# Kernel optimization log

Measured on AMD Instinct MI355X. Metric: run time of the kernel, lower is better.

## Reference

```python
import jax, jax.numpy as jnp
import numpy as np

HEADS = 8
DIM_HEAD = 64
SLICE = 64
DIM = 128
INNER = HEADS * DIM_HEAD
B, H, W = 4, 128, 128


def _conv(x_nchw, w_oihw, b):
    y = jax.lax.conv_general_dilated(
        x_nchw, w_oihw, window_strides=(1, 1), padding='SAME',
        dimension_numbers=('NCHW', 'OIHW', 'NCHW'))
    return y + b[None, :, None, None]


def setup_inputs() -> dict:
    key = jax.random.key(0)
    ks = jax.random.split(key, 10)
    s = lambda fan: 1.0 / np.sqrt(fan)
    return {
        'x': jax.random.normal(ks[0], (B, H, W, DIM), jnp.float32),
        'temperature': jnp.ones((1, HEADS, 1, 1), jnp.float32) * 0.5,
        'Wx': jax.random.normal(ks[1], (INNER, DIM, 3, 3), jnp.float32) * s(DIM * 9),
        'bx': jnp.zeros((INNER,), jnp.float32),
        'Wfx': jax.random.normal(ks[2], (INNER, DIM, 3, 3), jnp.float32) * s(DIM * 9),
        'bfx': jnp.zeros((INNER,), jnp.float32),
        'Ws': jax.random.normal(ks[3], (SLICE, DIM_HEAD), jnp.float32) * s(DIM_HEAD),
        'bs': jnp.zeros((SLICE,), jnp.float32),
        'Wq': jax.random.normal(ks[4], (DIM_HEAD, DIM_HEAD), jnp.float32) * s(DIM_HEAD),
        'Wk': jax.random.normal(ks[5], (DIM_HEAD, DIM_HEAD), jnp.float32) * s(DIM_HEAD),
        'Wv': jax.random.normal(ks[6], (DIM_HEAD, DIM_HEAD), jnp.float32) * s(DIM_HEAD),
        'Wo': jax.random.normal(ks[7], (DIM, INNER), jnp.float32) * s(INNER),
        'bo': jnp.zeros((DIM,), jnp.float32),
    }


def reference(x, temperature, Wx, bx, Wfx, bfx, Ws, bs, Wq, Wk, Wv, Wo, bo):
    b, h, w, _ = x.shape
    n = h * w
    scale = DIM_HEAD ** -0.5
    x_nchw = jnp.transpose(x, (0, 3, 1, 2))
    # conv projections -> [B, heads, N, dim_head]
    def to_heads(y):
        y = jnp.transpose(y, (0, 2, 3, 1)).reshape(b, n, HEADS, DIM_HEAD)
        return jnp.transpose(y, (0, 2, 1, 3))
    fx_mid = to_heads(_conv(x_nchw, Wfx, bfx))
    x_mid = to_heads(_conv(x_nchw, Wx, bx))
    # slice routing: softmax over M, temperature-scaled
    temp = jnp.clip(temperature, 0.1, 5.0)  # [1,heads,1,1]
    logits = (jnp.einsum('bhnc,gc->bhng', x_mid, Ws) + bs) / temp
    slice_weights = jax.nn.softmax(logits, axis=-1)  # [B,h,N,M]
    slice_norm = slice_weights.sum(axis=2)  # [B,h,M]
    slice_token = jnp.einsum('bhnc,bhng->bhgc', fx_mid, slice_weights)
    slice_token = slice_token / (slice_norm + 1e-5)[..., None]
    # small M x M attention over slice tokens
    q = jnp.einsum('bhgc,dc->bhgd', slice_token, Wq)
    k = jnp.einsum('bhgc,dc->bhgd', slice_token, Wk)
    v = jnp.einsum('bhgc,dc->bhgd', slice_token, Wv)
    dots = jnp.einsum('bhgd,bhkd->bhgk', q, k) * scale
    attn = jax.nn.softmax(dots, axis=-1)
    out_slice = jnp.einsum('bhgk,bhkd->bhgd', attn, v)
    # scatter back to points
    out_x = jnp.einsum('bhgc,bhng->bhnc', out_slice, slice_weights)
    out_x = jnp.transpose(out_x, (0, 2, 1, 3)).reshape(b, h, w, INNER)
    return jnp.einsum('bhwi,oi->bhwo', out_x, Wo) + bo
```

## Files before the change

### kernel.cpp

```cpp
#include <hip/hip_runtime.h>
#include <hip/hip_bf16.h>
#include <math.h>

#define B_ 4
#define H_ 128
#define W_ 128
#define DIM_ 128
#define HEADS_ 8
#define DH_ 64
#define G_ 64
#define INNER_ 512
#define N_ 16384

typedef __attribute__((ext_vector_type(8))) short sh8;
typedef __attribute__((ext_vector_type(4))) float vf4;

#define XPT_SLAB 4160
#define XPT_PLANE 2163200
#define WT_PLANE 1179648

__device__ __forceinline__ void gload16(const void* g, void* l) {
  __builtin_amdgcn_global_load_lds((const __attribute__((address_space(1))) void*)g,
                                   (__attribute__((address_space(3))) void*)l, 16, 0, 0);
}

__device__ __forceinline__ void split_bf16(float v, ushort& h, ushort& l) {
  __hip_bfloat16 hb = __float2bfloat16(v);
  float hf = __bfloat162float(hb);
  __hip_bfloat16 lb = __float2bfloat16(v - hf);
  h = *reinterpret_cast<ushort*>(&hb);
  l = *reinterpret_cast<ushort*>(&lb);
}

__global__ __launch_bounds__(256) void pad_tile_kernel(const float* __restrict__ x,
                                                       ushort* __restrict__ xpth,
                                                       ushort* __restrict__ xptl) {
  const int bz = blockIdx.y;
  x += (size_t)bz * N_ * DIM_;
  xpth += (size_t)bz * XPT_PLANE;
  xptl += (size_t)bz * XPT_PLANE;
  const int idx = blockIdx.x * 256 + threadIdx.x;
  const int row = idx / (4 * XPT_SLAB);
  const int rem = idx % (4 * XPT_SLAB);
  const int c0i = rem / XPT_SLAB;
  const int t2 = rem % XPT_SLAB;
  const int tile = t2 >> 3, j = t2 & 7;
  const int kg = tile / 130, px = tile % 130;
  const int c = c0i * 32 + kg * 8 + j;
  float v = 0.0f;
  if (row >= 1 && row <= H_ && px >= 1 && px <= W_)
    v = x[((size_t)(row - 1) * W_ + (px - 1)) * DIM_ + c];
  ushort hh, ll;
  split_bf16(v, hh, ll);
  xpth[idx] = hh;
  xptl[idx] = ll;
}

__global__ __launch_bounds__(256) void wfx_kernel(const float* __restrict__ Wfx,
                                                  ushort* __restrict__ wth,
                                                  ushort* __restrict__ wtl) {
  int idx = blockIdx.x * 256 + threadIdx.x;
  if (idx >= 9 * 512 * DIM_) return;
  const int c = idx & 127;
  const int ocf = (idx >> 7) & 511;
  const int tap = idx >> 16;
  float v = Wfx[((size_t)ocf * DIM_ + c) * 9 + tap];
  ushort hh, ll;
  split_bf16(v, hh, ll);
  const int nt = 4 + (ocf >> 7), oci = ocf & 127;
  const int c0i = c >> 5, kg = (c >> 3) & 3, j = c & 7;
  const size_t o = (((size_t)tap * 8 + nt) * 4 + c0i) * 4096 + ((size_t)kg * 128 + oci) * 8 + j;
  wth[o] = hh;
  wtl[o] = ll;
}

__global__ __launch_bounds__(256) void wcomp_kernel(const float* __restrict__ Wx,
                                                    const float* __restrict__ Ws,
                                                    const float* __restrict__ bx,
                                                    const float* __restrict__ bs,
                                                    const float* __restrict__ temperature,
                                                    ushort* __restrict__ wth,
                                                    ushort* __restrict__ wtl,
                                                    float* __restrict__ bc) {
  __shared__ float WxL[64][128];
  __shared__ float WsL[64][64];
  const int t = threadIdx.x;
  const int tap = blockIdx.x, h = blockIdx.y;
  for (int e = t; e < 8192; e += 256) {
    const int c2 = e >> 7, c = e & 127;
    WxL[c2][c] = Wx[((size_t)(h * 64 + c2) * DIM_ + c) * 9 + tap];
  }
  for (int e = t; e < 4096; e += 256) WsL[e >> 6][e & 63] = Ws[e];
  float tmp = fminf(fmaxf(temperature[h], 0.1f), 5.0f);
  const float invt = 1.0f / tmp;
  __syncthreads();
  for (int e = t; e < 8192; e += 256) {
    const int gg = e >> 7, c = e & 127;
    float s = 0.f;
#pragma unroll
    for (int c2 = 0; c2 < 64; ++c2) s = fmaf(WsL[gg][c2], WxL[c2][c], s);
    s *= invt;
    ushort hh, ll;
    split_bf16(s, hh, ll);
    const int ocp = h * 64 + gg;
    const int nt = ocp >> 7, oci = ocp & 127;
    const int c0i = c >> 5, kg = (c >> 3) & 3, j = c & 7;
    const size_t o = (((size_t)tap * 8 + nt) * 4 + c0i) * 4096 + ((size_t)kg * 128 + oci) * 8 + j;
    wth[o] = hh;
    wtl[o] = ll;
  }
  if (tap == 0 && t < 64) {
    float s = 0.f;
#pragma unroll
    for (int c2 = 0; c2 < 64; ++c2) s = fmaf(Ws[t * 64 + c2], bx[h * 64 + c2], s);
    bc[h * 64 + t] = (s + bs[t]) * invt;
  }
}

__global__ __launch_bounds__(256) void mqk_kernel(const float* __restrict__ Wq,
                                                  const float* __restrict__ Wk,
                                                  float* __restrict__ mqk) {
  const int idx = blockIdx.x * 256 + threadIdx.x;
  const int c = idx >> 6, c2 = idx & 63;
  float s = 0.f;
#pragma unroll
  for (int d = 0; d < 64; ++d) s = fmaf(Wq[d * 64 + c], Wk[d * 64 + c2], s);
  mqk[idx] = s * 0.125f;
}

__global__ __launch_bounds__(256) void conv_mfma_kernel(
    const ushort* __restrict__ xpth, const ushort* __restrict__ xptl,
    const ushort* __restrict__ wth, const ushort* __restrict__ wtl,
    const float* __restrict__ bc, const float* __restrict__ bfx,
    float* __restrict__ lg, float* __restrict__ fxo) {
  __shared__ __align__(16) ushort lds[24832];
  const int bz = blockIdx.z;
  xpth += (size_t)bz * XPT_PLANE;
  xptl += (size_t)bz * XPT_PLANE;
  lg += (size_t)bz * N_ * INNER_;
  fxo += (size_t)bz * N_ * INNER_;
  const int t = threadIdx.x;
  const int lane = t & 63;
  const int wid = t >> 6;
  const int wm = wid & 1, wn = wid >> 1;
  const int nt = blockIdx.x;
  const int y = blockIdx.y;
  const int col = lane & 15, quad = lane >> 4;

  vf4 acc[4][4];
#pragma unroll
  for (int i = 0; i < 4; ++i)
#pragma unroll
    for (int j = 0; j < 4; ++j) acc[i][j] = vf4{0.f, 0.f, 0.f, 0.f};

  auto stageA = [&](int p, int buf) {
    const int ky = p >> 2, c0i = p & 3;
    const size_t aoff = ((size_t)(y + ky) * 4 + c0i) * XPT_SLAB;
    const int base = buf * 8320;
    gload16(xpth + aoff + t * 8, lds + base + t * 8);
    gload16(xpth + aoff + 2048 + t * 8, lds + base + 2048 + t * 8);
    gload16(xptl + aoff + t * 8, lds + base + 4160 + t * 8);
    gload16(xptl + aoff + 2048 + t * 8, lds + base + 4160 + 2048 + t * 8);
    if (t < 8) {
      gload16(xpth + aoff + 4096 + t * 8, lds + base + 4096 + t * 8);
      gload16(xptl + aoff + 4096 + t * 8, lds + base + 4160 + 4096 + t * 8);
    }
  };
  auto stageB = [&](int p, int kx) {
    const int tap = (p >> 2) * 3 + kx;
    const int c0i = p & 3;
    const size_t boff = (((size_t)tap * 8 + nt) * 4 + c0i) * 4096;
    gload16(wth + boff + t * 8, lds + 16640 + t * 8);
    gload16(wth + boff + 2048 + t * 8, lds + 16640 + 2048 + t * 8);
    gload16(wtl + boff + t * 8, lds + 20736 + t * 8);
    gload16(wtl + boff + 2048 + t * 8, lds + 20736 + 2048 + t * 8);
  };

  stageA(0, 0);
  stageB(0, 0);
  __syncthreads();
  for (int p = 0; p < 12; ++p) {
    const int abase = (p & 1) * 8320;
    for (int kx = 0; kx < 3; ++kx) {
      sh8 ah[4], al[4], bh[4], bl[4];
#pragma unroll
      for (int j = 0; j < 4; ++j) {
        const int brd = (quad * 128 + wn * 64 + j * 16 + col) * 8;
        bh[j] = *reinterpret_cast<const sh8*>(lds + 16640 + brd);
        bl[j] = *reinterpret_cast<const sh8*>(lds + 20736 + brd);
      }
#pragma unroll
      for (int i = 0; i < 4; ++i) {
        const int ard = (quad * 130 + wm * 64 + i * 16 + col + kx) * 8;
        ah[i] = *reinterpret_cast<const sh8*>(lds + abase + ard);
        al[i] = *reinterpret_cast<const sh8*>(lds + abase + 4160 + ard);
      }
      const bool more = (kx < 2) || (p < 11);
      if (more) {
        __syncthreads();
        if (kx == 0 && p < 11) stageA(p + 1, (p + 1) & 1);
        if (kx < 2) stageB(p, kx + 1);
        else stageB(p + 1, 0);
      }
      __builtin_amdgcn_s_setprio(1);
#pragma unroll
      for (int i = 0; i < 4; ++i)
#pragma unroll
        for (int j = 0; j < 4; ++j) {
          acc[i][j] = __builtin_amdgcn_mfma_f32_16x16x32_bf16(ah[i], bh[j], acc[i][j], 0, 0, 0);
          acc[i][j] = __builtin_amdgcn_mfma_f32_16x16x32_bf16(ah[i], bl[j], acc[i][j], 0, 0, 0);
          acc[i][j] = __builtin_amdgcn_mfma_f32_16x16x32_bf16(al[i], bh[j], acc[i][j], 0, 0, 0);
        }
      __builtin_amdgcn_s_setprio(0);
      if (more) __syncthreads();
    }
  }
  const bool first = (nt < 4);
  float* outp = first ? lg : fxo;
  const float* bb = first ? bc : bfx;
  const int ocbase = (nt & 3) * 128 + wn * 64 + col;
#pragma unroll
  for (int j = 0; j < 4; ++j) {
    const int oc = ocbase + j * 16;
    const float bv = bb[oc];
#pragma unroll
    for (int i = 0; i < 4; ++i) {
#pragma unroll
      for (int r = 0; r < 4; ++r) {
        const int px = wm * 64 + i * 16 + quad * 4 + r;
        outp[((size_t)(y * W_ + px)) * INNER_ + oc] = acc[i][j][r] + bv;
      }
    }
  }
}

__device__ __forceinline__ void fma16(float (&acc)[4][4], const float4 a, const float4 b) {
  acc[0][0] = fmaf(a.x, b.x, acc[0][0]);
  acc[0][1] = fmaf(a.x, b.y, acc[0][1]);
  acc[0][2] = fmaf(a.x, b.z, acc[0][2]);
  acc[0][3] = fmaf(a.x, b.w, acc[0][3]);
  acc[1][0] = fmaf(a.y, b.x, acc[1][0]);
  acc[1][1] = fmaf(a.y, b.y, acc[1][1]);
  acc[1][2] = fmaf(a.y, b.z, acc[1][2]);
  acc[1][3] = fmaf(a.y, b.w, acc[1][3]);
  acc[2][0] = fmaf(a.z, b.x, acc[2][0]);
  acc[2][1] = fmaf(a.z, b.y, acc[2][1]);
  acc[2][2] = fmaf(a.z, b.z, acc[2][2]);
  acc[2][3] = fmaf(a.z, b.w, acc[2][3]);
  acc[3][0] = fmaf(a.w, b.x, acc[3][0]);
  acc[3][1] = fmaf(a.w, b.y, acc[3][1]);
  acc[3][2] = fmaf(a.w, b.z, acc[3][2]);
  acc[3][3] = fmaf(a.w, b.w, acc[3][3]);
}

__global__ __launch_bounds__(256) void slice_kernel(float* __restrict__ lg,
                                                    const float* __restrict__ fxg,
                                                    float* __restrict__ tpart,
                                                    float* __restrict__ npart) {
  __shared__ __align__(16) float wl[64][68];
  __shared__ __align__(16) float fxl[64][68];
  __shared__ float red[8][64];
  const int bz = blockIdx.y;
  lg += (size_t)bz * N_ * INNER_;
  fxg += (size_t)bz * N_ * INNER_;
  tpart += (size_t)bz * 512 * 4096;
  npart += (size_t)bz * 512 * 64;
  unsigned int* lgp = reinterpret_cast<unsigned int*>(lg);

  const int t = threadIdx.x;
  const int sub = blockIdx.x & 63;
  const int h = blockIdx.x >> 6;
  const int nbase = sub * 256;
  const int tx = t & 15;
  const int ty = t >> 4;
  const int sn = t >> 2;
  const int sq = t & 3;
  const int gg2 = t & 63;
  const int q2 = t >> 6;

  float acc2[4][4] = {};
  float snrmp = 0.0f;

  for (int s = 0; s < 4; ++s) {
    const int n0 = nbase + s * 64;
    __syncthreads();
    {
      const int cg = t & 15;
      const int nr = t >> 4;
#pragma unroll
      for (int r = 0; r < 4; ++r) {
        const int nn = nr + r * 16;
        const size_t rowoff = ((size_t)(n0 + nn)) * INNER_ + h * DH_ + cg * 4;
        *reinterpret_cast<float4*>(&wl[nn][cg * 4]) =
            *reinterpret_cast<const float4*>(lg + rowoff);
        *reinterpret_cast<float4*>(&fxl[nn][cg * 4]) =
            *reinterpret_cast<const float4*>(fxg + rowoff);
      }
    }
    __syncthreads();
    float m = -3.4e38f;
#pragma unroll
    for (int jj = 0; jj < 16; ++jj) m = fmaxf(m, wl[sn][sq * 16 + jj]);
    red[sq][sn] = m;
    __syncthreads();
    m = fmaxf(fmaxf(red[0][sn], red[1][sn]), fmaxf(red[2][sn], red[3][sn]));
    float ss = 0.0f;
#pragma unroll
    for (int jj = 0; jj < 16; ++jj) {
      const float e = __expf(wl[sn][sq * 16 + jj] - m);
      wl[sn][sq * 16 + jj] = e;
      ss += e;
    }
    red[4 + sq][sn] = ss;
    __syncthreads();
    const float inv = 1.0f / (red[4][sn] + red[5][sn] + red[6][sn] + red[7][sn]);
#pragma unroll
    for (int jj = 0; jj < 16; ++jj) wl[sn][sq * 16 + jj] *= inv;
    __syncthreads();
    {
      const int gg = t & 15;
      const int nr = t >> 4;
#pragma unroll
      for (int r = 0; r < 4; ++r) {
        const int nn = nr + r * 16;
        uint4 pk;
        unsigned int* pp = reinterpret_cast<unsigned int*>(&pk);
#pragma unroll
        for (int j = 0; j < 4; ++j) {
          ushort hh, ll;
          split_bf16(wl[nn][gg * 4 + j], hh, ll);
          pp[j] = ((unsigned int)hh << 16) | (unsigned int)ll;
        }
        *reinterpret_cast<uint4*>(lgp + ((size_t)(n0 + nn)) * INNER_ + h * DH_ + gg * 4) = pk;
      }
    }
#pragma unroll
    for (int nn = 0; nn < 16; ++nn) snrmp += wl[q2 * 16 + nn][gg2];
#pragma unroll
    for (int kk = 0; kk < 64; ++kk) {
      const float4 a4 = *reinterpret_cast<const float4*>(&wl[kk][ty * 4]);
      const float4 b4 = *reinterpret_cast<const float4*>(&fxl[kk][tx * 4]);
      fma16(acc2, a4, b4);
    }
  }
  __syncthreads();
  red[q2][gg2] = snrmp;
  float* tp = tpart + (size_t)blockIdx.x * 4096;
#pragma unroll
  for (int i = 0; i < 4; ++i) {
    float4 v;
    v.x = acc2[i][0];
    v.y = acc2[i][1];
    v.z = acc2[i][2];
    v.w = acc2[i][3];
    *reinterpret_cast<float4*>(tp + (ty * 4 + i) * 64 + tx * 4) = v;
  }
  __syncthreads();
  if (t < 64)
    npart[(size_t)blockIdx.x * 64 + t] = red[0][t] + red[1][t] + red[2][t] + red[3][t];
}

__global__ __launch_bounds__(256) void reduce_kernel(const float* __restrict__ tpart,
                                                     const float* __restrict__ npart,
                                                     float* __restrict__ tok,
                                                     float* __restrict__ nrm) {
  const int bz = blockIdx.y;
  tpart += (size_t)bz * 512 * 4096;
  npart += (size_t)bz * 512 * 64;
  tok += (size_t)bz * (HEADS_ * G_ * DH_);
  nrm += (size_t)bz * (HEADS_ * G_);
  if (blockIdx.x < 128) {
    const int idx = blockIdx.x * 256 + threadIdx.x;
    const int h = idx >> 12, e = idx & 4095;
    float s = 0.f;
    for (int cb = 0; cb < 64; ++cb)
      s += tpart[(((size_t)(h * 64 + cb)) << 12) + e];
    tok[idx] = s;
  } else {
    for (int o = threadIdx.x; o < 512; o += 256) {
      const int h = o >> 6, g = o & 63;
      float s = 0.f;
      for (int cb = 0; cb < 64; ++cb) s += npart[(size_t)(h * 64 + cb) * 64 + g];
      nrm[o] = s;
    }
  }
}

__global__ __launch_bounds__(256) void head_kernel(const float* __restrict__ tok,
                                                   const float* __restrict__ nrm,
                                                   const float* __restrict__ mqk,
                                                   const float* __restrict__ Wv,
                                                   const float* __restrict__ Wo,
                                                   ushort* __restrict__ mht,
                                                   ushort* __restrict__ mlt) {
  __shared__ float ST[64 * 65];
  __shared__ float YL[64 * 64];
  __shared__ float VL[64 * 64];
  __shared__ float red[8][64];
  const int bz = blockIdx.y;
  tok += (size_t)bz * (HEADS_ * G_ * DH_);
  nrm += (size_t)bz * (HEADS_ * G_);
  mht += (size_t)bz * (INNER_ * DIM_);
  mlt += (size_t)bz * (INNER_ * DIM_);
  const int t = threadIdx.x;
  const int h = blockIdx.x;

  for (int e = t; e < 4096; e += 256) {
    const int g = e >> 6, c = e & 63;
    ST[g * 65 + c] = tok[(size_t)h * 4096 + e] / (nrm[h * 64 + g] + 1e-5f);
  }
  __syncthreads();
  for (int e = t; e < 4096; e += 256) {
    const int k = e >> 6, c = e & 63;
    float sy = 0.f, sv = 0.f;
    const float* mrow = mqk + c * 64;
    const float* wrow = Wv + c * 64;
#pragma unroll
    for (int c2 = 0; c2 < 64; ++c2) {
      const float st2 = ST[k * 65 + c2];
      sy = fmaf(mrow[c2], st2, sy);
      sv = fmaf(wrow[c2], st2, sv);
    }
    YL[k * 64 + c] = sy;
    VL[k * 64 + c] = sv;
  }
  __syncthreads();
  const int g = t & 63, kp = t >> 6;
  float z[16];
#pragma unroll
  for (int j = 0; j < 16; ++j) z[j] = 0.f;
  for (int c = 0; c < 64; ++c) {
    const float sg = ST[g * 65 + c];
#pragma unroll
    for (int j = 0; j < 16; ++j) z[j] = fmaf(sg, YL[(kp * 16 + j) * 64 + c], z[j]);
  }
  float m = z[0];
#pragma unroll
  for (int j = 1; j < 16; ++j) m = fmaxf(m, z[j]);
  red[kp][g] = m;
  __syncthreads();
  m = fmaxf(fmaxf(red[0][g], red[1][g]), fmaxf(red[2][g], red[3][g]));
  float ssum = 0.f;
#pragma unroll
  for (int j = 0; j < 16; ++j) {
    z[j] = __expf(z[j] - m);
    ssum += z[j];
  }
  red[4 + kp][g] = ssum;
  __syncthreads();
  ssum = red[4][g] + red[5][g] + red[6][g] + red[7][g];
  const float inv = 1.f / ssum;
#pragma unroll
  for (int j = 0; j < 16; ++j) ST[(kp * 16 + j) * 65 + g] = z[j] * inv;
  __syncthreads();
  for (int e = t; e < 4096; e += 256) {
    const int gg = e >> 6, d = e & 63;
    float s = 0.f;
#pragma unroll
    for (int k = 0; k < 64; ++k) s = fmaf(ST[k * 65 + gg], VL[k * 64 + d], s);
    YL[gg * 64 + d] = s;
  }
  __syncthreads();
  for (int e = t; e < 8192; e += 256) {
    const int o = e & 127, gg = e >> 7;
    float s = 0.f;
    const float* wrow = Wo + (size_t)o * INNER_ + h * 64;
#pragma unroll
    for (int d = 0; d < 64; ++d) s = fmaf(YL[gg * 64 + d], wrow[d], s);
    ushort hh, ll;
    split_bf16(s, hh, ll);
    const int hg = h * 64 + gg;
    const int kg2 = hg >> 3, kr = hg & 7;
    mht[((size_t)kg2 * 128 + o) * 8 + kr] = hh;
    mlt[((size_t)kg2 * 128 + o) * 8 + kr] = ll;
  }
}

__global__ __launch_bounds__(256) void fused_out_kernel(
    const unsigned int* __restrict__ wp,
    const ushort* __restrict__ mht,
    const ushort* __restrict__ mlt,
    const float* __restrict__ bo,
    float* __restrict__ out) {
  __shared__ __align__(16) ushort lds[24576];
  const int bz = blockIdx.y;
  wp += (size_t)bz * N_ * INNER_;
  mht += (size_t)bz * (INNER_ * DIM_);
  mlt += (size_t)bz * (INNER_ * DIM_);
  out += (size_t)bz * N_ * DIM_;
  const int t = threadIdx.x;
  const int lane = t & 63;
  const int wid = t >> 6;
  const int wm = wid & 1, wn = wid >> 1;
  const int col = lane & 15, quad = lane >> 4;
  const int n0 = blockIdx.x * 64;

  vf4 acc[2][4];
#pragma unroll
  for (int m = 0; m < 2; ++m)
#pragma unroll
    for (int n = 0; n < 4; ++n) acc[m][n] = vf4{0.f, 0.f, 0.f, 0.f};

  for (int kc = 0; kc < 8; ++kc) {
    __syncthreads();
#pragma unroll
    for (int r = 0; r < 2; ++r) {
      const int row = r * 256 + t;
      const int pix = row >> 3, kg2 = row & 7;
      const unsigned int* gp = wp + (size_t)(n0 + pix) * INNER_ + kc * 64 + kg2 * 8;
      const uint4 p0 = *reinterpret_cast<const uint4*>(gp);
      const uint4 p1 = *reinterpret_cast<const uint4*>(gp + 4);
      unsigned int u[8] = {p0.x, p0.y, p0.z, p0.w, p1.x, p1.y, p1.z, p1.w};
      sh8 hv, lv;
#pragma unroll
      for (int j = 0; j < 8; ++j) {
        hv[j] = (short)(u[j] >> 16);
        lv[j] = (short)(u[j] & 0xffff);
      }
      const int drow = pix * 8 + (kg2 ^ (pix & 7));
      *reinterpret_cast<sh8*>(lds + drow * 8) = hv;
      *reinterpret_cast<sh8*>(lds + 4096 + drow * 8) = lv;
    }
#pragma unroll
    for (int r = 0; r < 4; ++r) {
      gload16(mht + (size_t)kc * 8192 + ((size_t)r * 256 + t) * 8, lds + 8192 + r * 2048 + t * 8);
      gload16(mlt + (size_t)kc * 8192 + ((size_t)r * 256 + t) * 8, lds + 16384 + r * 2048 + t * 8);
    }
    __syncthreads();
#pragma unroll
    for (int kk = 0; kk < 2; ++kk) {
      const int kg2 = kk * 4 + quad;
      sh8 ah[2], al[2], bh[4], bl[4];
#pragma unroll
      for (int m = 0; m < 2; ++m) {
        const int pix = wm * 32 + m * 16 + col;
        const int drow = pix * 8 + (kg2 ^ (pix & 7));
        ah[m] = *reinterpret_cast<const sh8*>(lds + drow * 8);
        al[m] = *reinterpret_cast<const sh8*>(lds + 4096 + drow * 8);
      }
#pragma unroll
      for (int n = 0; n < 4; ++n) {
        const int o = wn * 64 + n * 16 + col;
        bh[n] = *reinterpret_cast<const sh8*>(lds + 8192 + ((size_t)kg2 * 128 + o) * 8);
        bl[n] = *reinterpret_cast<const sh8*>(lds + 16384 + ((size_t)kg2 * 128 + o) * 8);
      }
      __builtin_amdgcn_s_setprio(1);
#pragma unroll
      for (int m = 0; m < 2; ++m)
#pragma unroll
        for (int n = 0; n < 4; ++n) {
          acc[m][n] = __builtin_amdgcn_mfma_f32_16x16x32_bf16(ah[m], bh[n], acc[m][n], 0, 0, 0);
          acc[m][n] = __builtin_amdgcn_mfma_f32_16x16x32_bf16(ah[m], bl[n], acc[m][n], 0, 0, 0);
          acc[m][n] = __builtin_amdgcn_mfma_f32_16x16x32_bf16(al[m], bh[n], acc[m][n], 0, 0, 0);
        }
      __builtin_amdgcn_s_setprio(0);
    }
  }
#pragma unroll
  for (int n = 0; n < 4; ++n) {
    const int o = wn * 64 + n * 16 + col;
    const float bv = bo[o];
#pragma unroll
    for (int m = 0; m < 2; ++m) {
#pragma unroll
      for (int r = 0; r < 4; ++r) {
        const int pix = wm * 32 + m * 16 + quad * 4 + r;
        out[(size_t)(n0 + pix) * DIM_ + o] = acc[m][n][r] + bv;
      }
    }
  }
}

extern "C" void kernel_launch(void* const* d_in, const int* in_sizes, int n_in,
                              void* d_out, int out_size, void* d_ws, size_t ws_size,
                              hipStream_t stream) {
  const float* x    = (const float*)d_in[0];
  const float* temp = (const float*)d_in[1];
  const float* Wx   = (const float*)d_in[2];
  const float* bx   = (const float*)d_in[3];
  const float* Wfx  = (const float*)d_in[4];
  const float* bfx  = (const float*)d_in[5];
  const float* Ws   = (const float*)d_in[6];
  const float* bs   = (const float*)d_in[7];
  const float* Wq   = (const float*)d_in[8];
  const float* Wk   = (const float*)d_in[9];
  const float* Wv   = (const float*)d_in[10];
  const float* Wo   = (const float*)d_in[11];
  const float* bo   = (const float*)d_in[12];
  float* out = (float*)d_out;

  auto need = [](int nb) -> size_t {
    size_t s = 0;
    s += 2 * (size_t)WT_PLANE * 2;
    s += 2 * (size_t)nb * XPT_PLANE * 2;
    s += 2 * (size_t)nb * N_ * INNER_ * 4;
    s += (size_t)B_ * HEADS_ * G_ * DH_ * 4;
    s += (size_t)B_ * HEADS_ * G_ * 4;
    s += (size_t)DH_ * DH_ * 4;
    s += (size_t)INNER_ * 4;
    s += 2 * (size_t)nb * INNER_ * DIM_ * 2;
    s += (size_t)nb * 512 * 4096 * 4;
    s += (size_t)nb * 512 * 64 * 4;
    return s;
  };
  int nb = 1;
  if (ws_size >= need(4)) nb = 4;
  else if (ws_size >= need(2)) nb = 2;

  char* p = (char*)d_ws;
  ushort* WTH = (ushort*)p; p += (size_t)WT_PLANE * 2;
  ushort* WTL = (ushort*)p; p += (size_t)WT_PLANE * 2;
  ushort* XPTH = (ushort*)p; p += (size_t)nb * XPT_PLANE * 2;
  ushort* XPTL = (ushort*)p; p += (size_t)nb * XPT_PLANE * 2;
  float* LG  = (float*)p; p += (size_t)nb * N_ * INNER_ * 4;
  float* FXO = (float*)p; p += (size_t)nb * N_ * INNER_ * 4;
  float* TOK = (float*)p; p += (size_t)B_ * HEADS_ * G_ * DH_ * 4;
  float* NRM = (float*)p; p += (size_t)B_ * HEADS_ * G_ * 4;
  float* MQK = (float*)p; p += (size_t)DH_ * DH_ * 4;
  float* BC  = (float*)p; p += (size_t)INNER_ * 4;
  ushort* MHT = (ushort*)p; p += (size_t)nb * INNER_ * DIM_ * 2;
  ushort* MLT = (ushort*)p; p += (size_t)nb * INNER_ * DIM_ * 2;
  float* TP  = (float*)p; p += (size_t)nb * 512 * 4096 * 4;
  float* NP  = (float*)p; p += (size_t)nb * 512 * 64 * 4;

  wfx_kernel<<<2304, 256, 0, stream>>>(Wfx, WTH, WTL);
  wcomp_kernel<<<dim3(9, 8), 256, 0, stream>>>(Wx, Ws, bx, bs, temp, WTH, WTL, BC);
  mqk_kernel<<<16, 256, 0, stream>>>(Wq, Wk, MQK);

  for (int b0 = 0; b0 < B_; b0 += nb) {
    const float* xb = x + (size_t)b0 * N_ * DIM_;
    float* outb = out + (size_t)b0 * N_ * DIM_;
    float* tokb = TOK + (size_t)b0 * HEADS_ * G_ * DH_;
    float* nrmb = NRM + (size_t)b0 * HEADS_ * G_;

    pad_tile_kernel<<<dim3(8450, nb), 256, 0, stream>>>(xb, XPTH, XPTL);
    conv_mfma_kernel<<<dim3(8, 128, nb), 256, 0, stream>>>(XPTH, XPTL, WTH, WTL, BC, bfx, LG, FXO);
    slice_kernel<<<dim3(512, nb), 256, 0, stream>>>(LG, FXO, TP, NP);
    reduce_kernel<<<dim3(129, nb), 256, 0, stream>>>(TP, NP, tokb, nrmb);
    head_kernel<<<dim3(8, nb), 256, 0, stream>>>(tokb, nrmb, MQK, Wv, Wo, MHT, MLT);
    fused_out_kernel<<<dim3(256, nb), 256, 0, stream>>>((const unsigned int*)LG, MHT, MLT, bo, outb);
  }
}
```

Before: 749.4 us.

## Load conv weight fragments directly from global instead of staging through LDS

The weight (B) operand tiles of the conv MFMA kernel are now read directly from global memory into registers instead of being staged through LDS with global_load_lds. This removes the per-kx B staging and two barriers per inner step, leaving one barrier per p iteration, and shrinks LDS use so more blocks can share a CU. The cost is exposed global/L2 latency on the B loads right before the MFMAs, with no prefetch to hide it. Each wave also re-fetches weights that were previously shared through LDS, which puts more load on the cache.

Result: slower. 769.5 us (+2.7%).

```diff
diff --git a/kernel.cpp b/kernel.cpp
--- a/kernel.cpp
+++ b/kernel.cpp
@@ -133,7 +133,7 @@
     const ushort* __restrict__ wth, const ushort* __restrict__ wtl,
     const float* __restrict__ bc, const float* __restrict__ bfx,
     float* __restrict__ lg, float* __restrict__ fxo) {
-  __shared__ __align__(16) ushort lds[24832];
+  __shared__ __align__(16) ushort lds[16640];
   const int bz = blockIdx.z;
   xpth += (size_t)bz * XPT_PLANE;
   xptl += (size_t)bz * XPT_PLANE;
@@ -166,41 +166,31 @@
       gload16(xptl + aoff + 4096 + t * 8, lds + base + 4160 + 4096 + t * 8);
     }
   };
-  auto stageB = [&](int p, int kx) {
-    const int tap = (p >> 2) * 3 + kx;
-    const int c0i = p & 3;
-    const size_t boff = (((size_t)tap * 8 + nt) * 4 + c0i) * 4096;
-    gload16(wth + boff + t * 8, lds + 16640 + t * 8);
-    gload16(wth + boff + 2048 + t * 8, lds + 16640 + 2048 + t * 8);
-    gload16(wtl + boff + t * 8, lds + 20736 + t * 8);
-    gload16(wtl + boff + 2048 + t * 8, lds + 20736 + 2048 + t * 8);
-  };
+
+  const int bfrag = (quad * 128 + wn * 64 + col) * 8;
 
   stageA(0, 0);
-  stageB(0, 0);
-  __syncthreads();
   for (int p = 0; p < 12; ++p) {
+    __syncthreads();
+    if (p < 11) stageA(p + 1, (p + 1) & 1);
     const int abase = (p & 1) * 8320;
+    const int tap0 = (p >> 2) * 3, c0i = p & 3;
+#pragma unroll
     for (int kx = 0; kx < 3; ++kx) {
+      const size_t boff = (((size_t)(tap0 + kx) * 8 + nt) * 4 + c0i) * 4096;
+      const ushort* __restrict__ bhp = wth + boff + bfrag;
+      const ushort* __restrict__ blp = wtl + boff + bfrag;
       sh8 ah[4], al[4], bh[4], bl[4];
 #pragma unroll
       for (int j = 0; j < 4; ++j) {
-        const int brd = (quad * 128 + wn * 64 + j * 16 + col) * 8;
-        bh[j] = *reinterpret_cast<const sh8*>(lds + 16640 + brd);
-        bl[j] = *reinterpret_cast<const sh8*>(lds + 20736 + brd);
+        bh[j] = *reinterpret_cast<const sh8*>(bhp + j * 128);
+        bl[j] = *reinterpret_cast<const sh8*>(blp + j * 128);
       }
 #pragma unroll
       for (int i = 0; i < 4; ++i) {
         const int ard = (quad * 130 + wm * 64 + i * 16 + col + kx) * 8;
         ah[i] = *reinterpret_cast<const sh8*>(lds + abase + ard);
         al[i] = *reinterpret_cast<const sh8*>(lds + abase + 4160 + ard);
-      }
-      const bool more = (kx < 2) || (p < 11);
-      if (more) {
-        __syncthreads();
-        if (kx == 0 && p < 11) stageA(p + 1, (p + 1) & 1);
-        if (kx < 2) stageB(p, kx + 1);
-        else stageB(p + 1, 0);
       }
       __builtin_amdgcn_s_setprio(1);
 #pragma unroll
@@ -212,7 +202,6 @@
           acc[i][j] = __builtin_amdgcn_mfma_f32_16x16x32_bf16(al[i], bh[j], acc[i][j], 0, 0, 0);
         }
       __builtin_amdgcn_s_setprio(0);
-      if (more) __syncthreads();
     }
   }
   const bool first = (nt < 4);
```
